# Kernel optimization log

Measured on AMD Instinct MI355X. Metric: run time of the kernel, lower is better.

Reference implementation:

```python
import jax, jax.numpy as jnp
import numpy as np

K_MASK = -2.3819763e+38
B, L, D = 2, 2048, 2048
NQ, NKV, H = 8, 4, 256
Q_SCALE = 0.0625  # head_dim ** -0.5
ROPE_BASE = 10000.0
SOFT_CAP = 50.0
WINDOW = 512
EPS = 1e-6


def apply_rope(x, positions, base=ROPE_BASE):
    # x: [B, L, N, H], positions: [B, L]; rope_proportion=1.0 -> no nope pad
    head_dim = x.shape[-1]
    half = head_dim // 2
    freq_exp = 2.0 / head_dim * jnp.arange(half, dtype=jnp.float32)
    timescale = base ** freq_exp                                   # [H/2]
    ang = positions[..., None].astype(jnp.float32) / timescale     # [B, L, H/2]
    ang = ang[..., None, :]                                        # [B, L, 1, H/2]
    sin, cos = jnp.sin(ang), jnp.cos(ang)
    x1, x2 = jnp.split(x, 2, axis=-1)
    out = jnp.concatenate([x1 * cos - x2 * sin, x2 * cos + x1 * sin], axis=-1)
    return out.astype(x.dtype)


def rms_norm(x, scale, eps=EPS):
    var = jnp.mean(jnp.square(x), axis=-1, keepdims=True)
    return x * jax.lax.rsqrt(var + eps) * (1.0 + scale)


def sliding_window_mask(positions, window):
    # bidirectional window: total size `window` split left/right
    q_pos = positions[:, :, None]
    k_pos = positions[:, None, :]
    dist = q_pos - k_pos
    left = (window + 1) // 2
    right = window // 2 + 1
    return ((dist >= 0) & (dist < left)) | ((dist < 0) & (-dist < right))  # [B, L, L]


def setup_inputs() -> dict:
    key = jax.random.key(0)
    ks = jax.random.split(key, 4)
    x = jax.random.normal(ks[0], (B, L, D), dtype=jnp.float32)
    segment_pos = jnp.tile(jnp.arange(L, dtype=jnp.int32)[None, :], (B, 1))
    attn_mask = jnp.ones((B, L, L), dtype=jnp.bool_)
    q_w = 0.01 * jax.random.normal(ks[1], (NQ, D, H), dtype=jnp.float32)
    kv_w = 0.01 * jax.random.normal(ks[2], (2, NKV, D, H), dtype=jnp.float32)
    o_w = 0.01 * jax.random.normal(ks[3], (NQ, H, D), dtype=jnp.float32)
    q_scale = jnp.zeros((H,), dtype=jnp.float32)
    k_scale = jnp.zeros((H,), dtype=jnp.float32)
    return {"x": x, "segment_pos": segment_pos, "attn_mask": attn_mask,
            "q_w": q_w, "kv_w": kv_w, "o_w": o_w,
            "q_scale": q_scale, "k_scale": k_scale}


def reference(x, segment_pos, attn_mask, q_w, kv_w, o_w, q_scale, k_scale):
    # projections (GQA path: num_kv_heads != num_q_heads)
    q = jnp.einsum('BTD,NDH->BTNH', x, q_w)                   # [B,T,NQ,H]
    kv = jnp.einsum('BSD,CKDH->CBSKH', x, kv_w)
    k, v = kv[0], kv[1]                                       # [B,S,NKV,H]
    # QK-RMSNorm
    q = rms_norm(q, q_scale)
    k = rms_norm(k, k_scale)
    # RoPE + query scaling
    q = apply_rope(q, segment_pos) * Q_SCALE
    k = apply_rope(k, segment_pos)
    # grouped logits
    G = NQ // NKV
    q = q.reshape(B, L, NKV, G, H)
    logits = jnp.einsum('BTKGH,BSKH->BTKGS', q, k).reshape(B, L, NQ, L)
    # soft cap
    logits = jnp.tanh(logits / SOFT_CAP) * SOFT_CAP
    # bidirectional sliding-window mask combined with attn_mask
    mask = attn_mask & sliding_window_mask(segment_pos, WINDOW)  # [B,L,L]
    padded = jnp.where(mask[:, :, None, :], logits, K_MASK)
    probs = jax.nn.softmax(padded, axis=-1).astype(k.dtype)
    probs = probs.reshape(B, L, NKV, G, L)
    enc = jnp.einsum('BTKGS,BSKH->BTKGH', probs, v).reshape(B, L, NQ, H)
    return jnp.einsum('BTNH,NHD->BTD', enc, o_w)
```

## Files before the change

### kernel.cpp

```cpp
#include <hip/hip_runtime.h>
#include <stdint.h>

#define B_   2
#define L_   2048
#define D_   2048
#define NQh  8
#define NKVh 4
#define H_   256

typedef __attribute__((ext_vector_type(8))) short bf16x8;
typedef __attribute__((ext_vector_type(4))) float f32x4;
typedef __attribute__((ext_vector_type(4))) unsigned short u16x4;

typedef __attribute__((address_space(1))) unsigned int as1_uint;
typedef __attribute__((address_space(3))) unsigned int as3_uint;

#define MFMA16(a, b, c) __builtin_amdgcn_mfma_f32_16x16x32_bf16((a), (b), (c), 0, 0, 0)

__device__ __forceinline__ unsigned short f2b(float f) {
  uint32_t u = __builtin_bit_cast(uint32_t, f);
  u += 0x7FFFu + ((u >> 16) & 1u);
  return (unsigned short)(u >> 16);
}
__device__ __forceinline__ float b2f(unsigned short s) {
  uint32_t u = (uint32_t)s << 16;
  return __builtin_bit_cast(float, u);
}

__device__ __forceinline__ void gload16(const unsigned short* g, unsigned short* l) {
  __builtin_amdgcn_global_load_lds((as1_uint*)g, (as3_uint*)l, 16, 0, 0);
}

template<int N> __device__ __forceinline__ void vmwait() {
  if constexpr (N == 8)      asm volatile("s_waitcnt vmcnt(8)" ::: "memory");
  else if constexpr (N == 6) asm volatile("s_waitcnt vmcnt(6)" ::: "memory");
  else if constexpr (N == 4) asm volatile("s_waitcnt vmcnt(4)" ::: "memory");
  else if constexpr (N == 3) asm volatile("s_waitcnt vmcnt(3)" ::: "memory");
  else                       asm volatile("s_waitcnt vmcnt(0)" ::: "memory");
}

__global__ void k_cvt_x(const float* __restrict__ x, unsigned short* __restrict__ xb) {
  int i = blockIdx.x * blockDim.x + threadIdx.x;
  float4 v = ((const float4*)x)[i];
  u16x4 o;
  o.x = f2b(v.x); o.y = f2b(v.y); o.z = f2b(v.z); o.w = f2b(v.w);
  ((u16x4*)xb)[i] = o;
}

__global__ void k_build_wt(const float* __restrict__ qw, const float* __restrict__ kvw,
                           unsigned short* __restrict__ Wt) {
  __shared__ float tile[32][33];
  int hb = blockIdx.z;
  int h0 = blockIdx.y * 32, d0 = blockIdx.x * 32;
  const float* src; int rowbase;
  if (hb < 8) { src = qw + (size_t)hb * D_ * H_;       rowbase = hb * 256; }
  else        { src = kvw + (size_t)(hb - 8) * D_ * H_; rowbase = 2048 + (hb - 8) * 256; }
  int tx = threadIdx.x & 31, ty = threadIdx.x >> 5;
  for (int i = 0; i < 4; i++) {
    int d = ty + i * 8;
    tile[d][tx] = src[(size_t)(d0 + d) * H_ + h0 + tx];
  }
  __syncthreads();
  for (int i = 0; i < 4; i++) {
    int h = ty + i * 8;
    Wt[(size_t)(rowbase + h0 + h) * D_ + d0 + tx] = f2b(tile[tx][h]);
  }
}

__global__ void k_build_owt(const float* __restrict__ ow, unsigned short* __restrict__ Owt) {
  __shared__ float tile[32][33];
  int r0 = blockIdx.y * 32, d0 = blockIdx.x * 32;
  int tx = threadIdx.x & 31, ty = threadIdx.x >> 5;
  for (int i = 0; i < 4; i++) {
    int r = ty + i * 8;
    tile[r][tx] = ow[(size_t)(r0 + r) * D_ + d0 + tx];
  }
  __syncthreads();
  for (int i = 0; i < 4; i++) {
    int d = ty + i * 8;
    Owt[(size_t)(d0 + d) * 2048 + r0 + tx] = f2b(tile[tx][d]);
  }
}

__global__ __launch_bounds__(512, 2) void k_gemm64(const unsigned short* __restrict__ A,
                                                   const unsigned short* __restrict__ Bt,
                                                   unsigned short* __restrict__ C,
                                                   int Ndim, int Kdim) {
  __shared__ __align__(16) unsigned short lds[65536];

  const int t = threadIdx.x;
  const int w = t >> 6, l = t & 63;
  const int wr = w >> 2, wc = w & 3;
  const int g = l >> 4, c = l & 15;
  const int m0 = blockIdx.y * 256, n0 = blockIdx.x * 256;
  const int NI = Kdim >> 7;

  const int chunk = ((l & 3) ^ ((l >> 3) & 3)) * 8;
  const unsigned short* Ag = A  + (size_t)(m0 + w * 16 + (l >> 2)) * Kdim + chunk;
  const unsigned short* Bg = Bt + (size_t)(n0 + w * 16 + (l >> 2)) * Kdim + chunk;
  const int rsw = (g ^ ((c >> 1) & 3)) * 8;

  auto stageA = [&](int kt, int ks) {
    unsigned short* dst = &lds[(kt & 1) * 32768 + ks * 8192 + w * 512];
    const unsigned short* src = Ag + (size_t)kt * 64 + ks * 32;
    gload16(src, dst);
    gload16(src + (size_t)128 * Kdim, dst + 4096);
  };
  auto stageB = [&](int kt, int ks) {
    unsigned short* dst = &lds[(kt & 1) * 32768 + 16384 + ks * 8192 + w * 512];
    const unsigned short* src = Bg + (size_t)kt * 64 + ks * 32;
    gload16(src, dst);
    gload16(src + (size_t)128 * Kdim, dst + 4096);
  };

  bf16x8 af[8];
  auto ldA = [&](int slot, int ks) {
#pragma unroll
    for (int m = 0; m < 8; m++)
      af[m] = *(const bf16x8*)&lds[slot * 32768 + ks * 8192 + (wr * 128 + m * 16 + c) * 32 + rsw];
  };
  auto ldB = [&](int slot, int ks, int n) {
    return *(const bf16x8*)&lds[slot * 32768 + 16384 + ks * 8192 + (wc * 64 + n * 16 + c) * 32 + rsw];
  };

  f32x4 acc[8][4] = {};

#define GPH(SLOT, KS, NH, DO_LDA, STAGE_STMT, VM_STMT)                        \
  {                                                                           \
    if (DO_LDA) ldA(SLOT, KS);                                                \
    bf16x8 b0 = ldB(SLOT, KS, (NH) * 2);                                      \
    bf16x8 b1 = ldB(SLOT, KS, (NH) * 2 + 1);                                  \
    STAGE_STMT;                                                               \
    __builtin_amdgcn_s_barrier();                                             \
    asm volatile("s_waitcnt lgkmcnt(0)" ::: "memory");                        \
    __builtin_amdgcn_s_setprio(1);                                            \
    _Pragma("unroll")                                                         \
    for (int m = 0; m < 8; m++) {                                             \
      acc[m][(NH) * 2]     = MFMA16(af[m], b0, acc[m][(NH) * 2]);             \
      acc[m][(NH) * 2 + 1] = MFMA16(af[m], b1, acc[m][(NH) * 2 + 1]);         \
    }                                                                         \
    __builtin_amdgcn_s_setprio(0);                                            \
    VM_STMT;                                                                  \
    __builtin_amdgcn_s_barrier();                                             \
  }

  stageA(0, 0); stageB(0, 0);
  stageA(0, 1); stageB(0, 1);
  stageA(1, 0); stageB(1, 0);
  vmwait<8>();
  __builtin_amdgcn_s_barrier();

  for (int i = 0; i < NI; i++) {
    const int ta = 2 * i, tb = 2 * i + 1;
    const bool nl = (i + 1 < NI);
    GPH(0, 0, 0, true,  { stageA(tb, 1); }, {});
    GPH(0, 0, 1, false, { stageB(tb, 1); }, { vmwait<8>(); });
    GPH(0, 1, 0, true,  { if (nl) stageA(ta + 2, 0); }, {});
    GPH(0, 1, 1, false, { if (nl) stageB(ta + 2, 0); },
        { if (nl) vmwait<8>(); else vmwait<4>(); });
    GPH(1, 0, 0, true,  { if (nl) stageA(ta + 2, 1); }, {});
    GPH(1, 0, 1, false, { if (nl) stageB(ta + 2, 1); },
        { if (nl) vmwait<8>(); else vmwait<0>(); });
    GPH(1, 1, 0, true,  { if (nl) stageA(tb + 2, 0); }, {});
    GPH(1, 1, 1, false, { if (nl) stageB(tb + 2, 0); }, { if (nl) vmwait<8>(); });
  }
#undef GPH

#pragma unroll
  for (int m = 0; m < 8; m++)
#pragma unroll
    for (int n = 0; n < 4; n++) {
      int row = m0 + wr * 128 + m * 16 + g * 4;
      int col = n0 + wc * 64 + n * 16 + c;
      unsigned short* cp = &C[(size_t)row * Ndim + col];
#pragma unroll
      for (int r = 0; r < 4; r++) cp[(size_t)r * Ndim] = f2b(acc[m][n][r]);
    }
}

template<int BM, int BN>
__global__ __launch_bounds__(512, 2) void k_gemm8p(const unsigned short* __restrict__ A,
                                                   const unsigned short* __restrict__ Bt,
                                                   float* __restrict__ C, int Ndim, int Kdim) {
  constexpr int MF  = BM / 32;
  constexpr int NF  = 4;
  constexpr int ASZ = BM * 32, BSZ = BN * 32;
  constexpr int SLOT = ASZ + BSZ;
  constexpr int LA  = BM / 128, LB = BN / 128;
  constexpr int U   = LA + LB;
  constexpr int NPH = (MF * NF) / 16;
  __shared__ __align__(16) unsigned short lds[4 * SLOT];

  const int t = threadIdx.x;
  const int w = t >> 6, l = t & 63;
  const int wr = w >> 2, wc = w & 3;
  const int g = l >> 4, c = l & 15;
  const int m0 = blockIdx.y * BM, n0 = blockIdx.x * BN;
  const int NT = Kdim >> 5;

  const int kswz = ((l & 3) ^ ((l >> 3) & 3)) * 8;
  const unsigned short* Ag = A  + (size_t)(m0 + w * 16 + (l >> 2)) * Kdim + kswz;
  const unsigned short* Bg = Bt + (size_t)(n0 + w * 16 + (l >> 2)) * Kdim + kswz;
  const int ldsA = w * 512;
  const int ldsB = ASZ + w * 512;
  const int gsw = (g ^ ((c >> 1) & 3)) * 8;

  auto stageA = [&](int kt) {
    int s = kt & 3;
#pragma unroll
    for (int j = 0; j < LA; j++)
      gload16(Ag + (size_t)j * 128 * Kdim + kt * 32, &lds[s * SLOT + ldsA + j * 4096]);
  };
  auto stageB = [&](int kt) {
    int s = kt & 3;
#pragma unroll
    for (int j = 0; j < LB; j++)
      gload16(Bg + (size_t)j * 128 * Kdim + kt * 32, &lds[s * SLOT + ldsB + j * 4096]);
  };

  f32x4 acc[MF][NF] = {};

  stageA(0); stageB(0);
  stageA(1); stageB(1);
  stageA(2); stageB(2);
  vmwait<2 * U>();
  __builtin_amdgcn_s_barrier();

  for (int i = 0; i < NT; i++) {
    const int s = i & 3;
    const unsigned short* As = &lds[s * SLOT];
    const unsigned short* Bs = &lds[s * SLOT + ASZ];
    bf16x8 af[MF];
#pragma unroll
    for (int m = 0; m < MF; m++)
      af[m] = *(const bf16x8*)&As[(wr * (BM / 2) + m * 16 + c) * 32 + gsw];

    if constexpr (NPH == 2) {
      bf16x8 bf0 = *(const bf16x8*)&Bs[(wc * 64 + 0 * 16 + c) * 32 + gsw];
      bf16x8 bf1 = *(const bf16x8*)&Bs[(wc * 64 + 1 * 16 + c) * 32 + gsw];
      if (i + 3 < NT) stageA(i + 3);
      __builtin_amdgcn_s_barrier();
      asm volatile("s_waitcnt lgkmcnt(0)" ::: "memory");
      __builtin_amdgcn_s_setprio(1);
#pragma unroll
      for (int m = 0; m < MF; m++) {
        acc[m][0] = MFMA16(af[m], bf0, acc[m][0]);
        acc[m][1] = MFMA16(af[m], bf1, acc[m][1]);
      }
      __builtin_amdgcn_s_setprio(0);
      __builtin_amdgcn_s_barrier();
      bf16x8 bf2 = *(const bf16x8*)&Bs[(wc * 64 + 2 * 16 + c) * 32 + gsw];
      bf16x8 bf3 = *(const bf16x8*)&Bs[(wc * 64 + 3 * 16 + c) * 32 + gsw];
      if (i + 3 < NT) stageB(i + 3);
      __builtin_amdgcn_s_barrier();
      asm volatile("s_waitcnt lgkmcnt(0)" ::: "memory");
      __builtin_amdgcn_s_setprio(1);
#pragma unroll
      for (int m = 0; m < MF; m++) {
        acc[m][2] = MFMA16(af[m], bf2, acc[m][2]);
        acc[m][3] = MFMA16(af[m], bf3, acc[m][3]);
      }
      __builtin_amdgcn_s_setprio(0);
      if (i < NT - 1) {
        int rem = NT - 2 - i;
        if (rem >= 2)      vmwait<2 * U>();
        else if (rem == 1) vmwait<U>();
        else               vmwait<0>();
      }
      __builtin_amdgcn_s_barrier();
    } else {
      bf16x8 bf[4];
#pragma unroll
      for (int n = 0; n < 4; n++)
        bf[n] = *(const bf16x8*)&Bs[(wc * 64 + n * 16 + c) * 32 + gsw];
      if (i + 3 < NT) { stageA(i + 3); stageB(i + 3); }
      __builtin_amdgcn_s_barrier();
      asm volatile("s_waitcnt lgkmcnt(0)" ::: "memory");
      __builtin_amdgcn_s_setprio(1);
#pragma unroll
      for (int m = 0; m < MF; m++)
#pragma unroll
        for (int n = 0; n < 4; n++)
          acc[m][n] = MFMA16(af[m], bf[n], acc[m][n]);
      __builtin_amdgcn_s_setprio(0);
      if (i < NT - 1) {
        int rem = NT - 2 - i;
        if (rem >= 2)      vmwait<2 * U>();
        else if (rem == 1) vmwait<U>();
        else               vmwait<0>();
      }
      __builtin_amdgcn_s_barrier();
    }
  }

#pragma unroll
  for (int m = 0; m < MF; m++)
#pragma unroll
    for (int n = 0; n < NF; n++) {
      int row = m0 + wr * (BM / 2) + m * 16 + g * 4;
      int col = n0 + wc * 64 + n * 16 + c;
      float* cp = &C[(size_t)row * Ndim + col];
#pragma unroll
      for (int r = 0; r < 4; r++) cp[(size_t)r * Ndim] = acc[m][n][r];
    }
}

__global__ __launch_bounds__(256) void k_postqk(const unsigned short* __restrict__ qkvb,
    const int* __restrict__ spos, const float* __restrict__ qs, const float* __restrict__ ks,
    unsigned short* __restrict__ qpre, unsigned short* __restrict__ kpre) {
  int wid = blockIdx.x * 4 + (threadIdx.x >> 6);
  int l = threadIdx.x & 63;
  int b, n, tpos, colbase; const float* scl; unsigned short* dst; float qmul;
  if (wid < B_ * NQh * L_) {
    b = wid / (NQh * L_); int rr = wid % (NQh * L_); n = rr / L_; tpos = rr % L_;
    colbase = n * 256; scl = qs; qmul = 0.0625f;
    dst = qpre + ((size_t)(b * NQh + n) * L_ + tpos) * H_;
  } else {
    int r2 = wid - B_ * NQh * L_;
    b = r2 / (NKVh * L_); int rr = r2 % (NKVh * L_); n = rr / L_; tpos = rr % L_;
    colbase = 2048 + n * 256; scl = ks; qmul = 1.0f;
    dst = kpre + ((size_t)(b * NKVh + n) * L_ + tpos) * H_;
  }
  const u16x4 v4 = *(const u16x4*)&qkvb[(size_t)(b * L_ + tpos) * 4096 + colbase + l * 4];
  float vv[4] = { b2f(v4.x), b2f(v4.y), b2f(v4.z), b2f(v4.w) };
  float ss = vv[0] * vv[0] + vv[1] * vv[1] + vv[2] * vv[2] + vv[3] * vv[3];
  for (int m = 1; m < 64; m <<= 1) ss += __shfl_xor(ss, m, 64);
  float inv = rsqrtf(ss * (1.0f / 256.0f) + 1e-6f);
  const float4 sc = *(const float4*)&scl[l * 4];
  float xv[4] = { vv[0] * inv * (1.f + sc.x), vv[1] * inv * (1.f + sc.y),
                  vv[2] * inv * (1.f + sc.z), vv[3] * inv * (1.f + sc.w) };
  float pf = (float)spos[b * L_ + tpos];
  u16x4 o;
#pragma unroll
  for (int i = 0; i < 4; i++) {
    int h = l * 4 + i, f = h & 127;
    float ts = __expf((float)f * (-9.210340371976184f / 128.0f));
    float ang = pf * ts;
    float s_, c_;
    __sincosf(ang, &s_, &c_);
    float part = __shfl_xor(xv[i], 32, 64);
    float r = (h < 128) ? (xv[i] * c_ - part * s_) : (xv[i] * c_ + part * s_);
    o[i] = f2b(r * qmul);
  }
  *(u16x4*)&dst[l * 4] = o;
}

__global__ void k_vtrans(const unsigned short* __restrict__ qkvb,
                         unsigned short* __restrict__ vpre) {
  __shared__ unsigned short tile[32][36];
  int bz = blockIdx.z; int b = bz >> 2, n = bz & 3;
  int t0 = blockIdx.x * 32, h0 = blockIdx.y * 32;
  int ty = threadIdx.x >> 3;
  int tx4 = (threadIdx.x & 7) * 4;
  *(u16x4*)&tile[ty][tx4] =
      *(const u16x4*)&qkvb[(size_t)(b * L_ + t0 + ty) * 4096 + 3072 + n * H_ + h0 + tx4];
  __syncthreads();
  size_t base = ((size_t)(b * NKVh + n) * 64 + (t0 >> 5)) * 8192;
  int hh = threadIdx.x >> 3;
  int tw4 = (threadIdx.x & 7) * 4;
  u16x4 o;
#pragma unroll
  for (int j = 0; j < 4; j++) o[j] = tile[tw4 + j][hh];
  *(u16x4*)&vpre[base + (size_t)(h0 + hh) * 32 + tw4] = o;
}

__global__ __launch_bounds__(256) void k_attn(const unsigned short* __restrict__ qpre,
    const unsigned short* __restrict__ kpre, const unsigned short* __restrict__ vpre,
    unsigned short* __restrict__ enc) {
  constexpr int KSZ = 32 * 264, VSZ = 256 * 40;
  __shared__ __align__(16) unsigned short Ksm[2 * KSZ];
  __shared__ __align__(16) unsigned short Vsm[2 * VSZ];
  int t = threadIdx.x;
  int wv = t >> 6, l = t & 63;
  int g = l >> 4, c = l & 15;
  int bid = blockIdx.x;
  int qt = bid & 31, n = (bid >> 5) & 7, b = bid >> 8;
  int t0 = qt * 64;
  int kv = n >> 1;
  int q = t0 + wv * 16 + c;

  const unsigned short* qb = qpre + ((size_t)(b * NQh + n) * L_ + t0 + wv * 16 + c) * H_;
  bf16x8 qf[8];
#pragma unroll
  for (int kk = 0; kk < 8; kk++) qf[kk] = *(const bf16x8*)&qb[kk * 32 + g * 8];

  const unsigned short* kh = kpre + (size_t)(b * NKVh + kv) * L_ * H_;
  const unsigned short* vh = vpre + (size_t)(b * NKVh + kv) * 64 * 8192;

  int ksrc = wv * 2048 + l * 8;
  int vsrc = wv * 2048 + l * 8;
  int kdst[4], vdst[4];
#pragma unroll
  for (int j = 0; j < 4; j++) {
    int krow = wv * 8 + j * 2 + (l >> 5);
    kdst[j] = krow * 264 + (l & 31) * 8;
    int vrow = wv * 64 + j * 16 + (l >> 2);
    vdst[j] = vrow * 40 + (l & 3) * 8;
  }

  f32x4 acc[16] = {};
  float lsum = 0.f;

  int c_lo = (t0 >= 256) ? 0 : ((256 - t0) >> 5);
  int c_hi = ((2272 - t0) >> 5) + 1; if (c_hi > 18) c_hi = 18;

  bf16x8 kreg[4], vreg[4];
  {
    int s0 = t0 - 256 + c_lo * 32;
    const unsigned short* kc = kh + (size_t)s0 * 256;
    const unsigned short* vc = vh + (size_t)(s0 >> 5) * 8192;
    int sl = c_lo & 1;
#pragma unroll
    for (int j = 0; j < 4; j++) {
      kreg[j] = *(const bf16x8*)&kc[ksrc + j * 512];
      vreg[j] = *(const bf16x8*)&vc[vsrc + j * 512];
    }
#pragma unroll
    for (int j = 0; j < 4; j++) {
      *(bf16x8*)&Ksm[sl * KSZ + kdst[j]] = kreg[j];
      *(bf16x8*)&Vsm[sl * VSZ + vdst[j]] = vreg[j];
    }
    __syncthreads();
  }

  for (int ci = c_lo; ci < c_hi; ci++) {
    int s0 = t0 - 256 + ci * 32;
    int sl = ci & 1;
    bool have_next = (ci + 1) < c_hi;
    if (have_next) {
      int s1 = s0 + 32;
      const unsigned short* kc = kh + (size_t)s1 * 256;
      const unsigned short* vc = vh + (size_t)(s1 >> 5) * 8192;
#pragma unroll
      for (int j = 0; j < 4; j++) {
        kreg[j] = *(const bf16x8*)&kc[ksrc + j * 512];
        vreg[j] = *(const bf16x8*)&vc[vsrc + j * 512];
      }
    }

    float p[2][4];
#pragma unroll
    for (int half = 0; half < 2; half++) {
      f32x4 st = {};
      __builtin_amdgcn_s_setprio(1);
#pragma unroll
      for (int kk = 0; kk < 8; kk++) {
        bf16x8 kf = *(const bf16x8*)&Ksm[sl * KSZ + (half * 16 + c) * 264 + kk * 32 + g * 8];
        st = MFMA16(kf, qf[kk], st);
      }
      __builtin_amdgcn_s_setprio(0);
#pragma unroll
      for (int r = 0; r < 4; r++) {
        int key = s0 + half * 16 + g * 4 + r;
        int d = key - q;
        bool valid = (d >= -255) && (d <= 256);
        float e1 = __expf(st[r] * 0.04f);
        float pe = __expf(fmaf(-100.f, __builtin_amdgcn_rcpf(e1 + 1.f), 40.f));
        float pv = valid ? pe : 0.f;
        p[half][r] = pv;
        lsum += pv;
      }
    }

    uint32_t pk[4];
#pragma unroll
    for (int r = 0; r < 4; r++)
      pk[r] = (uint32_t)f2b(p[0][r]) | ((uint32_t)f2b(p[1][r]) << 16);
    uint32_t rv[2][4];
#pragma unroll
    for (int jj = 0; jj < 2; jj++) {
      int srcl = (((l >> 4) & 1) * 2 + jj) * 16 + c;
#pragma unroll
      for (int r = 0; r < 4; r++)
        rv[jj][r] = (uint32_t)__shfl((int)pk[r], srcl, 64);
    }
    union { uint32_t u[4]; bf16x8 v8; } pb;
    int hi = g >> 1;
#pragma unroll
    for (int p2 = 0; p2 < 4; p2++) {
      uint32_t w0 = rv[p2 >> 1][(2 * p2) & 3];
      uint32_t w1 = rv[p2 >> 1][((2 * p2) & 3) + 1];
      uint32_t e0 = hi ? (w0 >> 16) : (w0 & 0xFFFFu);
      uint32_t e1 = hi ? (w1 >> 16) : (w1 & 0xFFFFu);
      pb.u[p2] = e0 | (e1 << 16);
    }
    __builtin_amdgcn_s_setprio(1);
#pragma unroll
    for (int ht = 0; ht < 16; ht++) {
      bf16x8 vf = *(const bf16x8*)&Vsm[sl * VSZ + (ht * 16 + c) * 40 + g * 8];
      acc[ht] = MFMA16(vf, pb.v8, acc[ht]);
    }
    __builtin_amdgcn_s_setprio(0);

    if (have_next) {
      int s2 = sl ^ 1;
#pragma unroll
      for (int j = 0; j < 4; j++) {
        *(bf16x8*)&Ksm[s2 * KSZ + kdst[j]] = kreg[j];
        *(bf16x8*)&Vsm[s2 * VSZ + vdst[j]] = vreg[j];
      }
    }
    __syncthreads();
  }

  lsum += __shfl_xor(lsum, 16, 64);
  lsum += __shfl_xor(lsum, 32, 64);
  float invl = 1.0f / lsum;
  unsigned short* eb = enc + ((size_t)(b * L_ + t0 + wv * 16 + c)) * 2048 + n * 256;
#pragma unroll
  for (int ht = 0; ht < 16; ht++) {
    u16x4 o;
#pragma unroll
    for (int r = 0; r < 4; r++) o[r] = f2b(acc[ht][r] * invl);
    *(u16x4*)&eb[ht * 16 + g * 4] = o;
  }
}

extern "C" void kernel_launch(void* const* d_in, const int* in_sizes, int n_in,
                              void* d_out, int out_size, void* d_ws, size_t ws_size,
                              hipStream_t stream) {
  const float* x   = (const float*)d_in[0];
  const int* spos  = (const int*)d_in[1];
  const float* qw  = (const float*)d_in[3];
  const float* kvw = (const float*)d_in[4];
  const float* ow  = (const float*)d_in[5];
  const float* qs  = (const float*)d_in[6];
  const float* ks  = (const float*)d_in[7];
  float* out = (float*)d_out;

  char* p = (char*)d_ws;
  unsigned short* xb   = (unsigned short*)p; p += (size_t)4096 * 2048 * 2;
  unsigned short* Wt   = (unsigned short*)p; p += (size_t)4096 * 2048 * 2;
  unsigned short* Owt  = (unsigned short*)p; p += (size_t)2048 * 2048 * 2;
  unsigned short* qkvb = (unsigned short*)p; p += (size_t)4096 * 4096 * 2;
  unsigned short* qpre = (unsigned short*)p; p += (size_t)B_ * NQh * L_ * H_ * 2;
  unsigned short* kpre = (unsigned short*)p; p += (size_t)B_ * NKVh * L_ * H_ * 2;
  unsigned short* vpre = (unsigned short*)p; p += (size_t)B_ * NKVh * L_ * H_ * 2;
  unsigned short* enc  = (unsigned short*)p; p += (size_t)4096 * 2048 * 2;

  k_cvt_x<<<8192, 256, 0, stream>>>(x, xb);
  k_build_wt<<<dim3(64, 8, 16), 256, 0, stream>>>(qw, kvw, Wt);
  k_build_owt<<<dim3(64, 64), 256, 0, stream>>>(ow, Owt);
  k_gemm64<<<dim3(16, 16), 512, 0, stream>>>(xb, Wt, qkvb, 4096, 2048);
  k_postqk<<<12288, 256, 0, stream>>>(qkvb, spos, qs, ks, qpre, kpre);
  k_vtrans<<<dim3(64, 8, 8), 256, 0, stream>>>(qkvb, vpre);
  k_attn<<<512, 256, 0, stream>>>(qpre, kpre, vpre, enc);
  k_gemm8p<128, 256><<<dim3(8, 32), 512, 0, stream>>>(enc, Owt, out, 2048, 2048);
}
```

Before: 192.9 us.

## Merge prep and post kernels; enlarge attention block to 128 queries

Fuses the three input-conversion kernels into one launch and the QK post-processing and V transpose into another, cutting launch count. The attention kernel now processes 128 queries per 512-thread block, so each staged K/V chunk is shared by twice as many waves. Waves whose 16 queries fall outside a chunk's window skip its MFMA work. The trade-off is half the grid size (256 blocks) and more chunk iterations per block, which may lower parallelism on a GPU with many CUs.

```diff
diff --git a/kernel.cpp b/kernel.cpp
--- a/kernel.cpp
+++ b/kernel.cpp
@@ -39,46 +39,48 @@
   else                       asm volatile("s_waitcnt vmcnt(0)" ::: "memory");
 }
 
-__global__ void k_cvt_x(const float* __restrict__ x, unsigned short* __restrict__ xb) {
-  int i = blockIdx.x * blockDim.x + threadIdx.x;
-  float4 v = ((const float4*)x)[i];
-  u16x4 o;
-  o.x = f2b(v.x); o.y = f2b(v.y); o.z = f2b(v.z); o.w = f2b(v.w);
-  ((u16x4*)xb)[i] = o;
-}
-
-__global__ void k_build_wt(const float* __restrict__ qw, const float* __restrict__ kvw,
-                           unsigned short* __restrict__ Wt) {
+__global__ __launch_bounds__(256) void k_prep(const float* __restrict__ x,
+    const float* __restrict__ qw, const float* __restrict__ kvw, const float* __restrict__ ow,
+    unsigned short* __restrict__ xb, unsigned short* __restrict__ Wt,
+    unsigned short* __restrict__ Owt) {
+  int bid = blockIdx.x;
+  if (bid < 8192) {
+    int i = bid * 256 + threadIdx.x;
+    float4 v = ((const float4*)x)[i];
+    u16x4 o;
+    o.x = f2b(v.x); o.y = f2b(v.y); o.z = f2b(v.z); o.w = f2b(v.w);
+    ((u16x4*)xb)[i] = o;
+    return;
+  }
   __shared__ float tile[32][33];
-  int hb = blockIdx.z;
-  int h0 = blockIdx.y * 32, d0 = blockIdx.x * 32;
-  const float* src; int rowbase;
-  if (hb < 8) { src = qw + (size_t)hb * D_ * H_;       rowbase = hb * 256; }
-  else        { src = kvw + (size_t)(hb - 8) * D_ * H_; rowbase = 2048 + (hb - 8) * 256; }
   int tx = threadIdx.x & 31, ty = threadIdx.x >> 5;
-  for (int i = 0; i < 4; i++) {
-    int d = ty + i * 8;
-    tile[d][tx] = src[(size_t)(d0 + d) * H_ + h0 + tx];
-  }
-  __syncthreads();
-  for (int i = 0; i < 4; i++) {
-    int h = ty + i * 8;
-    Wt[(size_t)(rowbase + h0 + h) * D_ + d0 + tx] = f2b(tile[tx][h]);
-  }
-}
-
-__global__ void k_build_owt(const float* __restrict__ ow, unsigned short* __restrict__ Owt) {
-  __shared__ float tile[32][33];
-  int r0 = blockIdx.y * 32, d0 = blockIdx.x * 32;
-  int tx = threadIdx.x & 31, ty = threadIdx.x >> 5;
-  for (int i = 0; i < 4; i++) {
-    int r = ty + i * 8;
-    tile[r][tx] = ow[(size_t)(r0 + r) * D_ + d0 + tx];
-  }
-  __syncthreads();
-  for (int i = 0; i < 4; i++) {
-    int d = ty + i * 8;
-    Owt[(size_t)(d0 + d) * 2048 + r0 + tx] = f2b(tile[tx][d]);
+  if (bid < 16384) {
+    int b2 = bid - 8192;
+    int d0 = (b2 & 63) * 32, h0 = ((b2 >> 6) & 7) * 32, hb = b2 >> 9;
+    const float* src; int rowbase;
+    if (hb < 8) { src = qw + (size_t)hb * D_ * H_;       rowbase = hb * 256; }
+    else        { src = kvw + (size_t)(hb - 8) * D_ * H_; rowbase = 2048 + (hb - 8) * 256; }
+    for (int i = 0; i < 4; i++) {
+      int d = ty + i * 8;
+      tile[d][tx] = src[(size_t)(d0 + d) * H_ + h0 + tx];
+    }
+    __syncthreads();
+    for (int i = 0; i < 4; i++) {
+      int h = ty + i * 8;
+      Wt[(size_t)(rowbase + h0 + h) * D_ + d0 + tx] = f2b(tile[tx][h]);
+    }
+  } else {
+    int b3 = bid - 16384;
+    int d0 = (b3 & 63) * 32, r0 = (b3 >> 6) * 32;
+    for (int i = 0; i < 4; i++) {
+      int r = ty + i * 8;
+      tile[r][tx] = ow[(size_t)(r0 + r) * D_ + d0 + tx];
+    }
+    __syncthreads();
+    for (int i = 0; i < 4; i++) {
+      int d = ty + i * 8;
+      Owt[(size_t)(d0 + d) * 2048 + r0 + tx] = f2b(tile[tx][d]);
+    }
   }
 }
 
@@ -305,51 +307,53 @@
     }
 }
 
-__global__ __launch_bounds__(256) void k_postqk(const unsigned short* __restrict__ qkvb,
+__global__ __launch_bounds__(256) void k_post(const unsigned short* __restrict__ qkvb,
     const int* __restrict__ spos, const float* __restrict__ qs, const float* __restrict__ ks,
-    unsigned short* __restrict__ qpre, unsigned short* __restrict__ kpre) {
-  int wid = blockIdx.x * 4 + (threadIdx.x >> 6);
-  int l = threadIdx.x & 63;
-  int b, n, tpos, colbase; const float* scl; unsigned short* dst; float qmul;
-  if (wid < B_ * NQh * L_) {
-    b = wid / (NQh * L_); int rr = wid % (NQh * L_); n = rr / L_; tpos = rr % L_;
-    colbase = n * 256; scl = qs; qmul = 0.0625f;
-    dst = qpre + ((size_t)(b * NQh + n) * L_ + tpos) * H_;
-  } else {
-    int r2 = wid - B_ * NQh * L_;
-    b = r2 / (NKVh * L_); int rr = r2 % (NKVh * L_); n = rr / L_; tpos = rr % L_;
-    colbase = 2048 + n * 256; scl = ks; qmul = 1.0f;
-    dst = kpre + ((size_t)(b * NKVh + n) * L_ + tpos) * H_;
-  }
-  const u16x4 v4 = *(const u16x4*)&qkvb[(size_t)(b * L_ + tpos) * 4096 + colbase + l * 4];
-  float vv[4] = { b2f(v4.x), b2f(v4.y), b2f(v4.z), b2f(v4.w) };
-  float ss = vv[0] * vv[0] + vv[1] * vv[1] + vv[2] * vv[2] + vv[3] * vv[3];
-  for (int m = 1; m < 64; m <<= 1) ss += __shfl_xor(ss, m, 64);
-  float inv = rsqrtf(ss * (1.0f / 256.0f) + 1e-6f);
-  const float4 sc = *(const float4*)&scl[l * 4];
-  float xv[4] = { vv[0] * inv * (1.f + sc.x), vv[1] * inv * (1.f + sc.y),
-                  vv[2] * inv * (1.f + sc.z), vv[3] * inv * (1.f + sc.w) };
-  float pf = (float)spos[b * L_ + tpos];
-  u16x4 o;
-#pragma unroll
-  for (int i = 0; i < 4; i++) {
-    int h = l * 4 + i, f = h & 127;
-    float ts = __expf((float)f * (-9.210340371976184f / 128.0f));
-    float ang = pf * ts;
-    float s_, c_;
-    __sincosf(ang, &s_, &c_);
-    float part = __shfl_xor(xv[i], 32, 64);
-    float r = (h < 128) ? (xv[i] * c_ - part * s_) : (xv[i] * c_ + part * s_);
-    o[i] = f2b(r * qmul);
-  }
-  *(u16x4*)&dst[l * 4] = o;
-}
-
-__global__ void k_vtrans(const unsigned short* __restrict__ qkvb,
-                         unsigned short* __restrict__ vpre) {
+    unsigned short* __restrict__ qpre, unsigned short* __restrict__ kpre,
+    unsigned short* __restrict__ vpre) {
+  int bid = blockIdx.x;
+  if (bid < 12288) {
+    int wid = bid * 4 + (threadIdx.x >> 6);
+    int l = threadIdx.x & 63;
+    int b, n, tpos, colbase; const float* scl; unsigned short* dst; float qmul;
+    if (wid < B_ * NQh * L_) {
+      b = wid / (NQh * L_); int rr = wid % (NQh * L_); n = rr / L_; tpos = rr % L_;
+      colbase = n * 256; scl = qs; qmul = 0.0625f;
+      dst = qpre + ((size_t)(b * NQh + n) * L_ + tpos) * H_;
+    } else {
+      int r2 = wid - B_ * NQh * L_;
+      b = r2 / (NKVh * L_); int rr = r2 % (NKVh * L_); n = rr / L_; tpos = rr % L_;
+      colbase = 2048 + n * 256; scl = ks; qmul = 1.0f;
+      dst = kpre + ((size_t)(b * NKVh + n) * L_ + tpos) * H_;
+    }
+    const u16x4 v4 = *(const u16x4*)&qkvb[(size_t)(b * L_ + tpos) * 4096 + colbase + l * 4];
+    float vv[4] = { b2f(v4.x), b2f(v4.y), b2f(v4.z), b2f(v4.w) };
+    float ss = vv[0] * vv[0] + vv[1] * vv[1] + vv[2] * vv[2] + vv[3] * vv[3];
+    for (int m = 1; m < 64; m <<= 1) ss += __shfl_xor(ss, m, 64);
+    float inv = rsqrtf(ss * (1.0f / 256.0f) + 1e-6f);
+    const float4 sc = *(const float4*)&scl[l * 4];
+    float xv[4] = { vv[0] * inv * (1.f + sc.x), vv[1] * inv * (1.f + sc.y),
+                    vv[2] * inv * (1.f + sc.z), vv[3] * inv * (1.f + sc.w) };
+    float pf = (float)spos[b * L_ + tpos];
+    u16x4 o;
+#pragma unroll
+    for (int i = 0; i < 4; i++) {
+      int h = l * 4 + i, f = h & 127;
+      float ts = __expf((float)f * (-9.210340371976184f / 128.0f));
+      float ang = pf * ts;
+      float s_, c_;
+      __sincosf(ang, &s_, &c_);
+      float part = __shfl_xor(xv[i], 32, 64);
+      float r = (h < 128) ? (xv[i] * c_ - part * s_) : (xv[i] * c_ + part * s_);
+      o[i] = f2b(r * qmul);
+    }
+    *(u16x4*)&dst[l * 4] = o;
+    return;
+  }
   __shared__ unsigned short tile[32][36];
-  int bz = blockIdx.z; int b = bz >> 2, n = bz & 3;
-  int t0 = blockIdx.x * 32, h0 = blockIdx.y * 32;
+  int b4 = bid - 12288;
+  int t0 = (b4 & 63) * 32, h0 = ((b4 >> 6) & 7) * 32;
+  int z = b4 >> 9; int b = z >> 2, n = z & 3;
   int ty = threadIdx.x >> 3;
   int tx4 = (threadIdx.x & 7) * 4;
   *(u16x4*)&tile[ty][tx4] =
@@ -364,7 +368,7 @@
   *(u16x4*)&vpre[base + (size_t)(h0 + hh) * 32 + tw4] = o;
 }
 
-__global__ __launch_bounds__(256) void k_attn(const unsigned short* __restrict__ qpre,
+__global__ __launch_bounds__(512, 4) void k_attn(const unsigned short* __restrict__ qpre,
     const unsigned short* __restrict__ kpre, const unsigned short* __restrict__ vpre,
     unsigned short* __restrict__ enc) {
   constexpr int KSZ = 32 * 264, VSZ = 256 * 40;
@@ -374,12 +378,13 @@
   int wv = t >> 6, l = t & 63;
   int g = l >> 4, c = l & 15;
   int bid = blockIdx.x;
-  int qt = bid & 31, n = (bid >> 5) & 7, b = bid >> 8;
-  int t0 = qt * 64;
+  int qt = bid & 15, n = (bid >> 4) & 7, b = bid >> 7;
+  int t0 = qt * 128;
   int kv = n >> 1;
-  int q = t0 + wv * 16 + c;
-
-  const unsigned short* qb = qpre + ((size_t)(b * NQh + n) * L_ + t0 + wv * 16 + c) * H_;
+  int qw0 = t0 + wv * 16;
+  int q = qw0 + c;
+
+  const unsigned short* qb = qpre + ((size_t)(b * NQh + n) * L_ + q) * H_;
   bf16x8 qf[8];
 #pragma unroll
   for (int kk = 0; kk < 8; kk++) qf[kk] = *(const bf16x8*)&qb[kk * 32 + g * 8];
@@ -387,36 +392,33 @@
   const unsigned short* kh = kpre + (size_t)(b * NKVh + kv) * L_ * H_;
   const unsigned short* vh = vpre + (size_t)(b * NKVh + kv) * 64 * 8192;
 
-  int ksrc = wv * 2048 + l * 8;
-  int vsrc = wv * 2048 + l * 8;
-  int kdst[4], vdst[4];
-#pragma unroll
-  for (int j = 0; j < 4; j++) {
-    int krow = wv * 8 + j * 2 + (l >> 5);
-    kdst[j] = krow * 264 + (l & 31) * 8;
-    int vrow = wv * 64 + j * 16 + (l >> 2);
-    vdst[j] = vrow * 40 + (l & 3) * 8;
+  int src0 = t * 8;
+  int kdst[2], vdst[2];
+#pragma unroll
+  for (int j = 0; j < 2; j++) {
+    kdst[j] = (j * 16 + (t >> 5)) * 264 + (t & 31) * 8;
+    vdst[j] = (j * 128 + (t >> 2)) * 40 + (t & 3) * 8;
   }
 
   f32x4 acc[16] = {};
   float lsum = 0.f;
 
   int c_lo = (t0 >= 256) ? 0 : ((256 - t0) >> 5);
-  int c_hi = ((2272 - t0) >> 5) + 1; if (c_hi > 18) c_hi = 18;
-
-  bf16x8 kreg[4], vreg[4];
+  int c_hi = ((2272 - t0) >> 5) + 1; if (c_hi > 20) c_hi = 20;
+
+  bf16x8 kreg[2], vreg[2];
   {
     int s0 = t0 - 256 + c_lo * 32;
     const unsigned short* kc = kh + (size_t)s0 * 256;
     const unsigned short* vc = vh + (size_t)(s0 >> 5) * 8192;
     int sl = c_lo & 1;
 #pragma unroll
-    for (int j = 0; j < 4; j++) {
-      kreg[j] = *(const bf16x8*)&kc[ksrc + j * 512];
-      vreg[j] = *(const bf16x8*)&vc[vsrc + j * 512];
-    }
-#pragma unroll
-    for (int j = 0; j < 4; j++) {
+    for (int j = 0; j < 2; j++) {
+      kreg[j] = *(const bf16x8*)&kc[src0 + j * 4096];
+      vreg[j] = *(const bf16x8*)&vc[src0 + j * 4096];
+    }
+#pragma unroll
+    for (int j = 0; j < 2; j++) {
       *(bf16x8*)&Ksm[sl * KSZ + kdst[j]] = kreg[j];
       *(bf16x8*)&Vsm[sl * VSZ + vdst[j]] = vreg[j];
     }
@@ -432,70 +434,73 @@
       const unsigned short* kc = kh + (size_t)s1 * 256;
       const unsigned short* vc = vh + (size_t)(s1 >> 5) * 8192;
 #pragma unroll
-      for (int j = 0; j < 4; j++) {
-        kreg[j] = *(const bf16x8*)&kc[ksrc + j * 512];
-        vreg[j] = *(const bf16x8*)&vc[vsrc + j * 512];
-      }
-    }
-
-    float p[2][4];
-#pragma unroll
-    for (int half = 0; half < 2; half++) {
-      f32x4 st = {};
+      for (int j = 0; j < 2; j++) {
+        kreg[j] = *(const bf16x8*)&kc[src0 + j * 4096];
+        vreg[j] = *(const bf16x8*)&vc[src0 + j * 4096];
+      }
+    }
+
+    bool active = (s0 + 31 >= qw0 - 255) && (s0 <= qw0 + 271);
+    if (active) {
+      float p[2][4];
+#pragma unroll
+      for (int half = 0; half < 2; half++) {
+        f32x4 st = {};
+        __builtin_amdgcn_s_setprio(1);
+#pragma unroll
+        for (int kk = 0; kk < 8; kk++) {
+          bf16x8 kf = *(const bf16x8*)&Ksm[sl * KSZ + (half * 16 + c) * 264 + kk * 32 + g * 8];
+          st = MFMA16(kf, qf[kk], st);
+        }
+        __builtin_amdgcn_s_setprio(0);
+#pragma unroll
+        for (int r = 0; r < 4; r++) {
+          int key = s0 + half * 16 + g * 4 + r;
+          int d = key - q;
+          bool valid = (d >= -255) && (d <= 256);
+          float e1 = __expf(st[r] * 0.04f);
+          float pe = __expf(fmaf(-100.f, __builtin_amdgcn_rcpf(e1 + 1.f), 40.f));
+          float pv = valid ? pe : 0.f;
+          p[half][r] = pv;
+          lsum += pv;
+        }
+      }
+
+      uint32_t pk[4];
+#pragma unroll
+      for (int r = 0; r < 4; r++)
+        pk[r] = (uint32_t)f2b(p[0][r]) | ((uint32_t)f2b(p[1][r]) << 16);
+      uint32_t rv[2][4];
+#pragma unroll
+      for (int jj = 0; jj < 2; jj++) {
+        int srcl = (((l >> 4) & 1) * 2 + jj) * 16 + c;
+#pragma unroll
+        for (int r = 0; r < 4; r++)
+          rv[jj][r] = (uint32_t)__shfl((int)pk[r], srcl, 64);
+      }
+      union { uint32_t u[4]; bf16x8 v8; } pb;
+      int hi = g >> 1;
+#pragma unroll
+      for (int p2 = 0; p2 < 4; p2++) {
+        uint32_t w0 = rv[p2 >> 1][(2 * p2) & 3];
+        uint32_t w1 = rv[p2 >> 1][((2 * p2) & 3) + 1];
+        uint32_t e0 = hi ? (w0 >> 16) : (w0 & 0xFFFFu);
+        uint32_t e1 = hi ? (w1 >> 16) : (w1 & 0xFFFFu);
+        pb.u[p2] = e0 | (e1 << 16);
+      }
       __builtin_amdgcn_s_setprio(1);
 #pragma unroll
-      for (int kk = 0; kk < 8; kk++) {
-        bf16x8 kf = *(const bf16x8*)&Ksm[sl * KSZ + (half * 16 + c) * 264 + kk * 32 + g * 8];
-        st = MFMA16(kf, qf[kk], st);
+      for (int ht = 0; ht < 16; ht++) {
+        bf16x8 vf = *(const bf16x8*)&Vsm[sl * VSZ + (ht * 16 + c) * 40 + g * 8];
+        acc[ht] = MFMA16(vf, pb.v8, acc[ht]);
       }
       __builtin_amdgcn_s_setprio(0);
-#pragma unroll
-      for (int r = 0; r < 4; r++) {
-        int key = s0 + half * 16 + g * 4 + r;
-        int d = key - q;
-        bool valid = (d >= -255) && (d <= 256);
-        float e1 = __expf(st[r] * 0.04f);
-        float pe = __expf(fmaf(-100.f, __builtin_amdgcn_rcpf(e1 + 1.f), 40.f));
-        float pv = valid ? pe : 0.f;
-        p[half][r] = pv;
-        lsum += pv;
-      }
-    }
-
-    uint32_t pk[4];
-#pragma unroll
-    for (int r = 0; r < 4; r++)
-      pk[r] = (uint32_t)f2b(p[0][r]) | ((uint32_t)f2b(p[1][r]) << 16);
-    uint32_t rv[2][4];
-#pragma unroll
-    for (int jj = 0; jj < 2; jj++) {
-      int srcl = (((l >> 4) & 1) * 2 + jj) * 16 + c;
-#pragma unroll
-      for (int r = 0; r < 4; r++)
-        rv[jj][r] = (uint32_t)__shfl((int)pk[r], srcl, 64);
-    }
-    union { uint32_t u[4]; bf16x8 v8; } pb;
-    int hi = g >> 1;
-#pragma unroll
-    for (int p2 = 0; p2 < 4; p2++) {
-      uint32_t w0 = rv[p2 >> 1][(2 * p2) & 3];
-      uint32_t w1 = rv[p2 >> 1][((2 * p2) & 3) + 1];
-      uint32_t e0 = hi ? (w0 >> 16) : (w0 & 0xFFFFu);
-      uint32_t e1 = hi ? (w1 >> 16) : (w1 & 0xFFFFu);
-      pb.u[p2] = e0 | (e1 << 16);
-    }
-    __builtin_amdgcn_s_setprio(1);
-#pragma unroll
-    for (int ht = 0; ht < 16; ht++) {
-      bf16x8 vf = *(const bf16x8*)&Vsm[sl * VSZ + (ht * 16 + c) * 40 + g * 8];
-      acc[ht] = MFMA16(vf, pb.v8, acc[ht]);
-    }
-    __builtin_amdgcn_s_setprio(0);
+    }
 
     if (have_next) {
       int s2 = sl ^ 1;
 #pragma unroll
-      for (int j = 0; j < 4; j++) {
+      for (int j = 0; j < 2; j++) {
         *(bf16x8*)&Ksm[s2 * KSZ + kdst[j]] = kreg[j];
         *(bf16x8*)&Vsm[s2 * VSZ + vdst[j]] = vreg[j];
       }
@@ -506,7 +511,7 @@
   lsum += __shfl_xor(lsum, 16, 64);
   lsum += __shfl_xor(lsum, 32, 64);
   float invl = 1.0f / lsum;
-  unsigned short* eb = enc + ((size_t)(b * L_ + t0 + wv * 16 + c)) * 2048 + n * 256;
+  unsigned short* eb = enc + ((size_t)(b * L_ + q)) * 2048 + n * 256;
 #pragma unroll
   for (int ht = 0; ht < 16; ht++) {
     u16x4 o;
@@ -538,12 +543,9 @@
   unsigned short* vpre = (unsigned short*)p; p += (size_t)B_ * NKVh * L_ * H_ * 2;
   unsigned short* enc  = (unsigned short*)p; p += (size_t)4096 * 2048 * 2;
 
-  k_cvt_x<<<8192, 256, 0, stream>>>(x, xb);
-  k_build_wt<<<dim3(64, 8, 16), 256, 0, stream>>>(qw, kvw, Wt);
-  k_build_owt<<<dim3(64, 64), 256, 0, stream>>>(ow, Owt);
+  k_prep<<<20480, 256, 0, stream>>>(x, qw, kvw, ow, xb, Wt, Owt);
   k_gemm64<<<dim3(16, 16), 512, 0, stream>>>(xb, Wt, qkvb, 4096, 2048);
-  k_postqk<<<12288, 256, 0, stream>>>(qkvb, spos, qs, ks, qpre, kpre);
-  k_vtrans<<<dim3(64, 8, 8), 256, 0, stream>>>(qkvb, vpre);
-  k_attn<<<512, 256, 0, stream>>>(qpre, kpre, vpre, enc);
+  k_post<<<16384, 256, 0, stream>>>(qkvb, spos, qs, ks, qpre, kpre, vpre);
+  k_attn<<<256, 512, 0, stream>>>(qpre, kpre, vpre, enc);
   k_gemm8p<128, 256><<<dim3(8, 32), 512, 0, stream>>>(enc, Owt, out, 2048, 2048);
 }
```

Result: slower. 250.4 us (+29.8%).
